# Kernel tuning notes

Hardware: AMD Instinct MI355X
Metric: run time of the kernel (lower is better)

The kernel has to match this reference:

```python
import jax, jax.numpy as jnp
import numpy as np

N_STEPS = 8


def _step(state, qop, dz_sub, W1, b1, W2, b2, W3, b3, W4, b4):
    # state [B,4], qop [B,1], dz_sub [B,1] -> residual-updated state [B,4]
    inp = jnp.concatenate([state, qop, dz_sub], axis=-1)  # [B,6]
    h = jax.nn.silu(inp @ W1 + b1)
    h = jax.nn.silu(h @ W2 + b2)
    h = jax.nn.silu(h @ W3 + b3)
    return state + (h @ W4 + b4)


def setup_inputs() -> dict:
    key = jax.random.key(0)
    ks = jax.random.split(key, 8)
    B = 262144
    H = 256
    # scale weights like xavier-ish init so activations stay sane
    def w(k, shape):
        fan_in = shape[0]
        return jax.random.normal(k, shape, dtype=jnp.float32) * (1.0 / np.sqrt(fan_in))
    state_dz = jax.random.normal(ks[0], (B, 6), dtype=jnp.float32)
    z_frac = jax.random.uniform(ks[1], (B,), dtype=jnp.float32)
    return {
        "state_dz": state_dz,
        "z_frac": z_frac,
        "W1": w(ks[2], (6, H)), "b1": jnp.zeros((H,), jnp.float32),
        "W2": w(ks[3], (H, H)), "b2": jnp.zeros((H,), jnp.float32),
        "W3": w(ks[4], (H, H)), "b3": jnp.zeros((H,), jnp.float32),
        "W4": w(ks[5], (H, 4)) * 0.1, "b4": jnp.zeros((4,), jnp.float32),
    }


def reference(state_dz, z_frac, W1, b1, W2, b2, W3, b3, W4, b4):
    # Faithful translation of CompositionalPINN.forward with z_frac of shape [B].
    # Torch uses max_steps = n_full.max().item() (host sync); running all N_STEPS
    # with the per-sample mask (n_full > step) yields identical math, since the
    # mask is 0 for step >= n_full.
    state = state_dz[:, :4]
    qop = state_dz[:, 4:5]
    dz_total = state_dz[:, 5:6]
    dz_sub = dz_total / N_STEPS

    continuous_steps = z_frac * N_STEPS            # [B]
    n_full = jnp.floor(continuous_steps)           # [B], kept float (compared vs step)
    frac_partial = continuous_steps - n_full       # [B]

    for step in range(N_STEPS):
        mask = (n_full > step).astype(state.dtype)[:, None]  # [B,1]
        new_state = _step(state, qop, dz_sub, W1, b1, W2, b2, W3, b3, W4, b4)
        state = mask * new_state + (1.0 - mask) * state

    dz_partial = frac_partial[:, None] * dz_sub
    has_partial = (frac_partial > 1e-6).astype(state.dtype)[:, None]
    partial_state = _step(state, qop, dz_partial, W1, b1, W2, b2, W3, b3, W4, b4)
    state = has_partial * partial_state + (1.0 - has_partial) * state
    return state
```

## Files before the change

kernel.cpp:

```cpp
#include <hip/hip_runtime.h>

typedef unsigned short u16;
typedef unsigned int u32;
typedef __attribute__((ext_vector_type(8))) short v8s;
typedef __attribute__((ext_vector_type(4))) float f32x4;

#define RPB 64
#define THREADS 256
#define NSB 512
#define W1F 0
#define W2F 8192
#define W3F 73728
#define W4F 139264
#define TOTW 143360
#define BH_OFF 286720
#define PERM_OFF 305152

#define MFMA(w, b, c) __builtin_amdgcn_mfma_f32_16x16x32_bf16((w), (b), (c), 0, 0, 0)

typedef __attribute__((address_space(1))) const unsigned int gu32;
typedef __attribute__((address_space(3))) unsigned int su32;
__device__ __forceinline__ void gld16(const u16* g, u16* l) {
  __builtin_amdgcn_global_load_lds((gu32*)g, (su32*)l, 16, 0, 0);
}

__device__ __forceinline__ u32 pk2(float a, float b) {
  u32 r;
  asm("v_cvt_pk_bf16_f32 %0, %1, %2" : "=v"(r) : "v"(a), "v"(b));
  return r;
}
__device__ __forceinline__ float bfu(u32 w, int hi) {
  return __uint_as_float(hi ? (w & 0xffff0000u) : (w << 16));
}
__device__ __forceinline__ f32x4 silu4(f32x4 v) {
  f32x4 r;
#pragma unroll
  for (int i = 0; i < 4; ++i) r[i] = v[i] * __builtin_amdgcn_rcpf(1.0f + __expf(-v[i]));
  return r;
}

__global__ void prep_weights(const float* __restrict__ W1, const float* __restrict__ W2,
                             const float* __restrict__ W3, const float* __restrict__ W4,
                             u16* __restrict__ Wf) {
  int e = blockIdx.x * 256 + threadIdx.x;
  if (e >= TOTW) return;
  float val = 0.0f;
  if (e < W2F) {
    int mt = e >> 9, idx = e & 511, l = idx >> 3, j = idx & 7;
    int q = l >> 4, m = l & 15;
    int f = 16 * (j >> 2) + 4 * q + (j & 3);
    int col = mt * 16 + m;
    val = (f < 6) ? W1[f * 256 + col] : ((f < 12) ? W1[(f - 6) * 256 + col] : 0.0f);
  } else if (e < W3F) {
    int e2 = e - W2F, blk = e2 >> 9, idx = e2 & 511, l = idx >> 3, j = idx & 7;
    int ks = blk >> 4, mt = blk & 15, q = l >> 4, m = l & 15;
    int f = 32 * ks + 16 * (j >> 2) + 4 * q + (j & 3);
    val = W2[f * 256 + mt * 16 + m];
  } else if (e < W4F) {
    int e2 = e - W3F, blk = e2 >> 9, idx = e2 & 511, l = idx >> 3, j = idx & 7;
    int ks = blk >> 4, mt = blk & 15, q = l >> 4, m = l & 15;
    int f = 32 * ks + 16 * (j >> 2) + 4 * q + (j & 3);
    val = W3[f * 256 + mt * 16 + m];
  } else {
    int e2 = e - W4F, ks = e2 >> 9, idx = e2 & 511, l = idx >> 3, j = idx & 7;
    int q = l >> 4, m = l & 15;
    int f = 32 * ks + 16 * (j >> 2) + 4 * q + (j & 3);
    val = (m < 4) ? W4[f * 4 + m] : 0.0f;
  }
  Wf[e] = (u16)pk2(val, val);
}

__global__ void hist_blocks(const float* __restrict__ zf, int* __restrict__ bh, int B) {
  __shared__ int h[9];
  int t = threadIdx.x;
  if (t < 9) h[t] = 0;
  __syncthreads();
  int r = blockIdx.x * 512 + t;
  if (r < B) {
    int nf = min(max((int)floorf(zf[r] * 8.0f), 0), 8);
    atomicAdd(&h[nf], 1);
  }
  __syncthreads();
  if (t < 9) bh[blockIdx.x * 9 + t] = h[t];
}

__global__ void scan_offsets(int* __restrict__ bh) {
  __shared__ int S[NSB * 9];
  __shared__ int tot[9], ebase[9];
  int t = threadIdx.x;
  for (int i = t; i < NSB * 9; i += 512) S[i] = bh[i];
  __syncthreads();
  if (t < 9) {
    int s = 0;
    for (int b = 0; b < NSB; ++b) s += S[b * 9 + t];
    tot[t] = s;
  }
  __syncthreads();
  if (t == 0) {
    int s = 0;
    for (int i = 0; i < 9; ++i) { ebase[i] = s; s += tot[i]; }
  }
  __syncthreads();
  if (t < 9) {
    int off = ebase[t];
    for (int b = 0; b < NSB; ++b) { int c = S[b * 9 + t]; S[b * 9 + t] = off; off += c; }
  }
  __syncthreads();
  for (int i = t; i < NSB * 9; i += 512) bh[i] = S[i];
}

__global__ void scatter_sorted(const float* __restrict__ zf, const int* __restrict__ bh,
                               int* __restrict__ perm, int B) {
  __shared__ int off[9];
  int t = threadIdx.x;
  if (t < 9) off[t] = bh[blockIdx.x * 9 + t];
  __syncthreads();
  int r = blockIdx.x * 512 + t;
  if (r < B) {
    int nf = min(max((int)floorf(zf[r] * 8.0f), 0), 8);
    int pos = atomicAdd(&off[nf], 1);
    perm[pos] = r;
  }
}

__global__ __attribute__((amdgpu_flat_work_group_size(256, 256)))
__attribute__((amdgpu_waves_per_eu(2, 2))) void pinn_main(
    const float* __restrict__ sdz, const float* __restrict__ zf,
    const u16* __restrict__ Wf, const int* __restrict__ perm,
    const float* __restrict__ b1, const float* __restrict__ b2,
    const float* __restrict__ b3, const float* __restrict__ b4,
    float* __restrict__ out) {
  __shared__ __align__(16) u16 ringS[4][4096];
  __shared__ __align__(16) u16 W1s[8192];
  __shared__ __align__(16) u16 W4s[4096];
  __shared__ __align__(16) float biasS[784];
  __shared__ __align__(16) float stS[RPB * 4];
  __shared__ float qopS[RPB], dzS[RPB], fracS[RPB];
  __shared__ int nfS[RPB], rowG[RPB];

  const int t = threadIdx.x;
  const int lane = t & 63;
  const int q = lane >> 4;
  const int n = lane & 15;
  const int wv = t >> 6;
  const int rb = wv * 16;

  if (t < RPB) {
    int rg = perm[blockIdx.x * RPB + t];
    rowG[t] = rg;
    const float* p = sdz + (size_t)rg * 6;
    stS[t * 4 + 0] = p[0]; stS[t * 4 + 1] = p[1];
    stS[t * 4 + 2] = p[2]; stS[t * 4 + 3] = p[3];
    qopS[t] = p[4];
    dzS[t] = p[5] * 0.125f;
    float cs = zf[rg] * 8.0f;
    float nfl = floorf(cs);
    nfS[t] = (int)nfl;
    fracS[t] = cs - nfl;
  }
  biasS[t] = b1[t]; biasS[256 + t] = b2[t]; biasS[512 + t] = b3[t];
  if (t < 16) biasS[768 + t] = (t < 4) ? b4[t] : 0.0f;
#pragma unroll
  for (int c = 0; c < 4; ++c)
    gld16(Wf + W1F + (c * 4 + wv) * 512 + lane * 8, &W1s[(c * 4 + wv) * 512]);
#pragma unroll
  for (int c = 0; c < 2; ++c)
    gld16(Wf + W4F + (c * 4 + wv) * 512 + lane * 8, &W4s[(c * 4 + wv) * 512]);
  __syncthreads();
  const int maxnf = nfS[RPB - 1];

  f32x4 acc[16];
  v8s bact[8];

#define ISSUE_HALF(AP)                                                        \
  do {                                                                        \
    int p_ = (AP) & 31;                                                       \
    int off_ = ((p_ >> 4) ? W3F : W2F) + ((p_ >> 1) & 7) * 8192 + (p_ & 1) * 4096; \
    u16* dst_ = &ringS[(AP) & 3][0];                                          \
    gld16(Wf + off_ + (2 * wv) * 512 + lane * 8, dst_ + (2 * wv) * 512);      \
    gld16(Wf + off_ + (2 * wv + 1) * 512 + lane * 8, dst_ + (2 * wv + 1) * 512); \
  } while (0)

  int ap = 0;
  ISSUE_HALF(ap);
  ISSUE_HALF(ap + 1);

#define PACK_BACT()                                              \
  do {                                                           \
    _Pragma("unroll") for (int ks = 0; ks < 8; ++ks) {           \
      f32x4 a0 = silu4(acc[2 * ks]);                             \
      f32x4 a1 = silu4(acc[2 * ks + 1]);                         \
      union { int4 i; v8s s; } u_;                               \
      u_.i.x = (int)pk2(a0[0], a0[1]);                           \
      u_.i.y = (int)pk2(a0[2], a0[3]);                           \
      u_.i.z = (int)pk2(a1[0], a1[1]);                           \
      u_.i.w = (int)pk2(a1[2], a1[3]);                           \
      bact[ks] = u_.s;                                           \
    }                                                            \
  } while (0)

  for (int ev = 0; ev <= maxnf; ++ev) {
    const bool partial = (ev == maxnf);

    v8s b1f;
    {
      const int row = rb + n;
      const float4 st = *(const float4*)&stS[row * 4];
      const float qop = qopS[row];
      const float dzv = partial ? fracS[row] * dzS[row] : dzS[row];
      u32 h01 = pk2(st.x, st.y), h23 = pk2(st.z, st.w), hqd = pk2(qop, dzv);
      float l0 = st.x - bfu(h01, 0), l1 = st.y - bfu(h01, 1);
      float l2 = st.z - bfu(h23, 0), l3 = st.w - bfu(h23, 1);
      float lq = qop - bfu(hqd, 0), ld = dzv - bfu(hqd, 1);
      u32 w0 = 0, w1 = 0;
      if (q == 0) { w0 = h01; w1 = h23; }
      else if (q == 1) { w0 = hqd; w1 = pk2(l0, l1); }
      else if (q == 2) { w0 = pk2(l2, l3); w1 = pk2(lq, ld); }
      union { int4 i; v8s s; } u_;
      u_.i.x = (int)w0; u_.i.y = (int)w1; u_.i.z = 0; u_.i.w = 0;
      b1f = u_.s;
    }

#pragma unroll
    for (int mt = 0; mt < 16; ++mt) {
      const v8s w = *(const v8s*)&W1s[mt * 512 + lane * 8];
      const float4 bb = *(const float4*)&biasS[mt * 16 + q * 4];
      const f32x4 binit = {bb.x, bb.y, bb.z, bb.w};
      acc[mt] = MFMA(w, b1f, binit);
    }
    PACK_BACT();

#pragma unroll
    for (int layer = 0; layer < 2; ++layer) {
      const int Lb = (layer == 0) ? 256 : 512;
#pragma unroll
      for (int mt = 0; mt < 16; ++mt) {
        const float4 bb = *(const float4*)&biasS[Lb + mt * 16 + q * 4];
        const f32x4 binit = {bb.x, bb.y, bb.z, bb.w};
        acc[mt] = binit;
      }
#pragma unroll
      for (int ks = 0; ks < 8; ++ks) {
#pragma unroll
        for (int h = 0; h < 2; ++h) {
          ISSUE_HALF(ap + 2);
          asm volatile("s_waitcnt vmcnt(4)" ::: "memory");
          __builtin_amdgcn_sched_barrier(0);
          __builtin_amdgcn_s_barrier();
          __builtin_amdgcn_sched_barrier(0);
          asm volatile("" ::: "memory");
          const u16* buf = &ringS[ap & 3][0];
          __builtin_amdgcn_s_setprio(1);
#pragma unroll
          for (int i = 0; i < 8; ++i) {
            const v8s w = *(const v8s*)&buf[i * 512 + lane * 8];
            acc[h * 8 + i] = MFMA(w, bact[ks], acc[h * 8 + i]);
          }
          __builtin_amdgcn_s_setprio(0);
          ++ap;
        }
      }
      PACK_BACT();
    }

    {
      const float4 bb = *(const float4*)&biasS[768 + q * 4];
      f32x4 a4 = {bb.x, bb.y, bb.z, bb.w};
#pragma unroll
      for (int ks = 0; ks < 8; ++ks) {
        const v8s w = *(const v8s*)&W4s[ks * 512 + lane * 8];
        a4 = MFMA(w, bact[ks], a4);
      }
      if (q == 0) {
        const int row = rb + n;
        const bool act = partial ? (fracS[row] > 1e-6f) : (nfS[row] > ev);
        if (act) {
          float4 cur = *(float4*)&stS[row * 4];
          cur.x += a4[0]; cur.y += a4[1];
          cur.z += a4[2]; cur.w += a4[3];
          *(float4*)&stS[row * 4] = cur;
        }
      }
    }
  }
  __syncthreads();

  {
    const int i = t;
    out[(size_t)rowG[i >> 2] * 4 + (i & 3)] = stS[i];
  }
}

extern "C" void kernel_launch(void* const* d_in, const int* in_sizes, int n_in,
                              void* d_out, int out_size, void* d_ws, size_t ws_size,
                              hipStream_t stream) {
  const float* sdz = (const float*)d_in[0];
  const float* zfr = (const float*)d_in[1];
  const float* W1 = (const float*)d_in[2];
  const float* b1 = (const float*)d_in[3];
  const float* W2 = (const float*)d_in[4];
  const float* b2 = (const float*)d_in[5];
  const float* W3 = (const float*)d_in[6];
  const float* b3 = (const float*)d_in[7];
  const float* W4 = (const float*)d_in[8];
  const float* b4 = (const float*)d_in[9];

  char* ws = (char*)d_ws;
  u16* Wf = (u16*)ws;
  int* bh = (int*)(ws + BH_OFF);
  int* perm = (int*)(ws + PERM_OFF);

  const int B = in_sizes[1];

  prep_weights<<<(TOTW + 255) / 256, 256, 0, stream>>>(W1, W2, W3, W4, Wf);
  hist_blocks<<<NSB, 512, 0, stream>>>(zfr, bh, B);
  scan_offsets<<<1, 512, 0, stream>>>(bh);
  scatter_sorted<<<NSB, 512, 0, stream>>>(zfr, bh, perm, B);
  pinn_main<<<B / RPB, THREADS, 0, stream>>>(sdz, zfr, Wf, perm, b1, b2, b3, b4,
                                             (float*)d_out);
}
```

Measured before the change: 549.8 us.

## Switch to 32x32x16 bf16 MFMA with 128 rows per block

```diff
diff --git a/kernel.cpp b/kernel.cpp
--- a/kernel.cpp
+++ b/kernel.cpp
@@ -3,20 +3,20 @@
 typedef unsigned short u16;
 typedef unsigned int u32;
 typedef __attribute__((ext_vector_type(8))) short v8s;
-typedef __attribute__((ext_vector_type(4))) float f32x4;
-
-#define RPB 64
+typedef __attribute__((ext_vector_type(16))) float f32x16;
+
+#define RPB 128
 #define THREADS 256
 #define NSB 512
 #define W1F 0
-#define W2F 8192
-#define W3F 73728
-#define W4F 139264
+#define W2F 4096
+#define W3F 69632
+#define W4F 135168
 #define TOTW 143360
 #define BH_OFF 286720
 #define PERM_OFF 305152
 
-#define MFMA(w, b, c) __builtin_amdgcn_mfma_f32_16x16x32_bf16((w), (b), (c), 0, 0, 0)
+#define MFMA32(w, b, c) __builtin_amdgcn_mfma_f32_32x32x16_bf16((w), (b), (c), 0, 0, 0)
 
 typedef __attribute__((address_space(1))) const unsigned int gu32;
 typedef __attribute__((address_space(3))) unsigned int su32;
@@ -32,11 +32,8 @@
 __device__ __forceinline__ float bfu(u32 w, int hi) {
   return __uint_as_float(hi ? (w & 0xffff0000u) : (w << 16));
 }
-__device__ __forceinline__ f32x4 silu4(f32x4 v) {
-  f32x4 r;
-#pragma unroll
-  for (int i = 0; i < 4; ++i) r[i] = v[i] * __builtin_amdgcn_rcpf(1.0f + __expf(-v[i]));
-  return r;
+__device__ __forceinline__ float silu1(float x) {
+  return x * __builtin_amdgcn_rcpf(1.0f + __expf(-x));
 }
 
 __global__ void prep_weights(const float* __restrict__ W1, const float* __restrict__ W2,
@@ -47,24 +44,24 @@
   float val = 0.0f;
   if (e < W2F) {
     int mt = e >> 9, idx = e & 511, l = idx >> 3, j = idx & 7;
-    int q = l >> 4, m = l & 15;
-    int f = 16 * (j >> 2) + 4 * q + (j & 3);
-    int col = mt * 16 + m;
+    int g = l >> 5, m = l & 31;
+    int f = ((j >> 2) << 3) + (g << 2) + (j & 3);
+    int col = mt * 32 + m;
     val = (f < 6) ? W1[f * 256 + col] : ((f < 12) ? W1[(f - 6) * 256 + col] : 0.0f);
   } else if (e < W3F) {
     int e2 = e - W2F, blk = e2 >> 9, idx = e2 & 511, l = idx >> 3, j = idx & 7;
-    int ks = blk >> 4, mt = blk & 15, q = l >> 4, m = l & 15;
-    int f = 32 * ks + 16 * (j >> 2) + 4 * q + (j & 3);
-    val = W2[f * 256 + mt * 16 + m];
+    int s = blk >> 3, mt = blk & 7, g = l >> 5, m = l & 31;
+    int f = ((s >> 1) << 5) + ((s & 1) << 4) + ((j >> 2) << 3) + (g << 2) + (j & 3);
+    val = W2[f * 256 + mt * 32 + m];
   } else if (e < W4F) {
     int e2 = e - W3F, blk = e2 >> 9, idx = e2 & 511, l = idx >> 3, j = idx & 7;
-    int ks = blk >> 4, mt = blk & 15, q = l >> 4, m = l & 15;
-    int f = 32 * ks + 16 * (j >> 2) + 4 * q + (j & 3);
-    val = W3[f * 256 + mt * 16 + m];
+    int s = blk >> 3, mt = blk & 7, g = l >> 5, m = l & 31;
+    int f = ((s >> 1) << 5) + ((s & 1) << 4) + ((j >> 2) << 3) + (g << 2) + (j & 3);
+    val = W3[f * 256 + mt * 32 + m];
   } else {
-    int e2 = e - W4F, ks = e2 >> 9, idx = e2 & 511, l = idx >> 3, j = idx & 7;
-    int q = l >> 4, m = l & 15;
-    int f = 32 * ks + 16 * (j >> 2) + 4 * q + (j & 3);
+    int e2 = e - W4F, s = e2 >> 9, idx = e2 & 511, l = idx >> 3, j = idx & 7;
+    int g = l >> 5, m = l & 31;
+    int f = ((s >> 1) << 5) + ((s & 1) << 4) + ((j >> 2) << 3) + (g << 2) + (j & 3);
     val = (m < 4) ? W4[f * 4 + m] : 0.0f;
   }
   Wf[e] = (u16)pk2(val, val);
@@ -131,19 +128,20 @@
     const float* __restrict__ b3, const float* __restrict__ b4,
     float* __restrict__ out) {
   __shared__ __align__(16) u16 ringS[4][4096];
-  __shared__ __align__(16) u16 W1s[8192];
-  __shared__ __align__(16) u16 W4s[4096];
-  __shared__ __align__(16) float biasS[784];
+  __shared__ __align__(16) u16 W1s[4096];
+  __shared__ __align__(16) u16 W4s[8192];
+  __shared__ __align__(16) float biasS[800];
   __shared__ __align__(16) float stS[RPB * 4];
   __shared__ float qopS[RPB], dzS[RPB], fracS[RPB];
   __shared__ int nfS[RPB], rowG[RPB];
 
   const int t = threadIdx.x;
   const int lane = t & 63;
-  const int q = lane >> 4;
-  const int n = lane & 15;
+  const int g = lane >> 5;
+  const int g4 = g << 2;
+  const int n32 = lane & 31;
   const int wv = t >> 6;
-  const int rb = wv * 16;
+  const int rb = wv * 32;
 
   if (t < RPB) {
     int rg = perm[blockIdx.x * RPB + t];
@@ -159,44 +157,60 @@
     fracS[t] = cs - nfl;
   }
   biasS[t] = b1[t]; biasS[256 + t] = b2[t]; biasS[512 + t] = b3[t];
-  if (t < 16) biasS[768 + t] = (t < 4) ? b4[t] : 0.0f;
+  if (t < 32) biasS[768 + t] = (t < 4) ? b4[t] : 0.0f;
+#pragma unroll
+  for (int c = 0; c < 2; ++c)
+    gld16(Wf + W1F + (c * 4 + wv) * 512 + lane * 8, &W1s[(c * 4 + wv) * 512]);
 #pragma unroll
   for (int c = 0; c < 4; ++c)
-    gld16(Wf + W1F + (c * 4 + wv) * 512 + lane * 8, &W1s[(c * 4 + wv) * 512]);
-#pragma unroll
-  for (int c = 0; c < 2; ++c)
     gld16(Wf + W4F + (c * 4 + wv) * 512 + lane * 8, &W4s[(c * 4 + wv) * 512]);
   __syncthreads();
   const int maxnf = nfS[RPB - 1];
 
-  f32x4 acc[16];
-  v8s bact[8];
-
-#define ISSUE_HALF(AP)                                                        \
+  f32x16 acc[8];
+  v8s bact[16];
+
+#define ISSUE_SLICE(AP)                                                       \
   do {                                                                        \
     int p_ = (AP) & 31;                                                       \
-    int off_ = ((p_ >> 4) ? W3F : W2F) + ((p_ >> 1) & 7) * 8192 + (p_ & 1) * 4096; \
+    int off_ = ((p_ >> 4) ? W3F : W2F) + (p_ & 15) * 4096;                    \
     u16* dst_ = &ringS[(AP) & 3][0];                                          \
     gld16(Wf + off_ + (2 * wv) * 512 + lane * 8, dst_ + (2 * wv) * 512);      \
     gld16(Wf + off_ + (2 * wv + 1) * 512 + lane * 8, dst_ + (2 * wv + 1) * 512); \
   } while (0)
 
   int ap = 0;
-  ISSUE_HALF(ap);
-  ISSUE_HALF(ap + 1);
-
-#define PACK_BACT()                                              \
-  do {                                                           \
-    _Pragma("unroll") for (int ks = 0; ks < 8; ++ks) {           \
-      f32x4 a0 = silu4(acc[2 * ks]);                             \
-      f32x4 a1 = silu4(acc[2 * ks + 1]);                         \
-      union { int4 i; v8s s; } u_;                               \
-      u_.i.x = (int)pk2(a0[0], a0[1]);                           \
-      u_.i.y = (int)pk2(a0[2], a0[3]);                           \
-      u_.i.z = (int)pk2(a1[0], a1[1]);                           \
-      u_.i.w = (int)pk2(a1[2], a1[3]);                           \
-      bact[ks] = u_.s;                                           \
-    }                                                            \
+  ISSUE_SLICE(ap);
+  ISSUE_SLICE(ap + 1);
+
+#define PACK_BACT()                                                 \
+  do {                                                              \
+    _Pragma("unroll") for (int mt = 0; mt < 8; ++mt) {              \
+      float s_[16];                                                 \
+      _Pragma("unroll") for (int i = 0; i < 16; ++i)                \
+          s_[i] = silu1(acc[mt][i]);                                \
+      union { int4 i4; v8s v; } lo_, hi_;                           \
+      lo_.i4.x = (int)pk2(s_[0], s_[1]);                            \
+      lo_.i4.y = (int)pk2(s_[2], s_[3]);                            \
+      lo_.i4.z = (int)pk2(s_[4], s_[5]);                            \
+      lo_.i4.w = (int)pk2(s_[6], s_[7]);                            \
+      hi_.i4.x = (int)pk2(s_[8], s_[9]);                            \
+      hi_.i4.y = (int)pk2(s_[10], s_[11]);                          \
+      hi_.i4.z = (int)pk2(s_[12], s_[13]);                          \
+      hi_.i4.w = (int)pk2(s_[14], s_[15]);                          \
+      bact[2 * mt] = lo_.v;                                         \
+      bact[2 * mt + 1] = hi_.v;                                     \
+    }                                                               \
+  } while (0)
+
+#define BINIT(BI, LB, MT)                                           \
+  do {                                                              \
+    _Pragma("unroll") for (int rq = 0; rq < 4; ++rq) {              \
+      const float4 bb =                                             \
+          *(const float4*)&biasS[(LB) + (MT) * 32 + rq * 8 + g4];   \
+      (BI)[4 * rq + 0] = bb.x; (BI)[4 * rq + 1] = bb.y;             \
+      (BI)[4 * rq + 2] = bb.z; (BI)[4 * rq + 3] = bb.w;             \
+    }                                                               \
   } while (0)
 
   for (int ev = 0; ev <= maxnf; ++ev) {
@@ -204,7 +218,7 @@
 
     v8s b1f;
     {
-      const int row = rb + n;
+      const int row = rb + n32;
       const float4 st = *(const float4*)&stS[row * 4];
       const float qop = qopS[row];
       const float dzv = partial ? fracS[row] * dzS[row] : dzS[row];
@@ -212,21 +226,23 @@
       float l0 = st.x - bfu(h01, 0), l1 = st.y - bfu(h01, 1);
       float l2 = st.z - bfu(h23, 0), l3 = st.w - bfu(h23, 1);
       float lq = qop - bfu(hqd, 0), ld = dzv - bfu(hqd, 1);
-      u32 w0 = 0, w1 = 0;
-      if (q == 0) { w0 = h01; w1 = h23; }
-      else if (q == 1) { w0 = hqd; w1 = pk2(l0, l1); }
-      else if (q == 2) { w0 = pk2(l2, l3); w1 = pk2(lq, ld); }
-      union { int4 i; v8s s; } u_;
-      u_.i.x = (int)w0; u_.i.y = (int)w1; u_.i.z = 0; u_.i.w = 0;
-      b1f = u_.s;
+      union { int4 i4; v8s v; } u_;
+      if (g == 0) {
+        u_.i4.x = (int)h01; u_.i4.y = (int)h23;
+        u_.i4.z = (int)pk2(l2, l3); u_.i4.w = (int)pk2(lq, ld);
+      } else {
+        u_.i4.x = (int)hqd; u_.i4.y = (int)pk2(l0, l1);
+        u_.i4.z = 0; u_.i4.w = 0;
+      }
+      b1f = u_.v;
     }
 
 #pragma unroll
-    for (int mt = 0; mt < 16; ++mt) {
+    for (int mt = 0; mt < 8; ++mt) {
       const v8s w = *(const v8s*)&W1s[mt * 512 + lane * 8];
-      const float4 bb = *(const float4*)&biasS[mt * 16 + q * 4];
-      const f32x4 binit = {bb.x, bb.y, bb.z, bb.w};
-      acc[mt] = MFMA(w, b1f, binit);
+      f32x16 bi;
+      BINIT(bi, 0, mt);
+      acc[mt] = MFMA32(w, b1f, bi);
     }
     PACK_BACT();
 
@@ -234,45 +250,47 @@
     for (int layer = 0; layer < 2; ++layer) {
       const int Lb = (layer == 0) ? 256 : 512;
 #pragma unroll
-      for (int mt = 0; mt < 16; ++mt) {
-        const float4 bb = *(const float4*)&biasS[Lb + mt * 16 + q * 4];
-        const f32x4 binit = {bb.x, bb.y, bb.z, bb.w};
-        acc[mt] = binit;
-      }
-#pragma unroll
-      for (int ks = 0; ks < 8; ++ks) {
-#pragma unroll
-        for (int h = 0; h < 2; ++h) {
-          ISSUE_HALF(ap + 2);
-          asm volatile("s_waitcnt vmcnt(4)" ::: "memory");
-          __builtin_amdgcn_sched_barrier(0);
-          __builtin_amdgcn_s_barrier();
-          __builtin_amdgcn_sched_barrier(0);
-          asm volatile("" ::: "memory");
-          const u16* buf = &ringS[ap & 3][0];
-          __builtin_amdgcn_s_setprio(1);
-#pragma unroll
-          for (int i = 0; i < 8; ++i) {
-            const v8s w = *(const v8s*)&buf[i * 512 + lane * 8];
-            acc[h * 8 + i] = MFMA(w, bact[ks], acc[h * 8 + i]);
-          }
-          __builtin_amdgcn_s_setprio(0);
-          ++ap;
+      for (int mt = 0; mt < 8; ++mt) {
+        f32x16 bi;
+        BINIT(bi, Lb, mt);
+        acc[mt] = bi;
+      }
+#pragma unroll
+      for (int s = 0; s < 16; ++s) {
+        ISSUE_SLICE(ap + 2);
+        asm volatile("s_waitcnt vmcnt(4)" ::: "memory");
+        __builtin_amdgcn_sched_barrier(0);
+        __builtin_amdgcn_s_barrier();
+        __builtin_amdgcn_sched_barrier(0);
+        asm volatile("" ::: "memory");
+        const u16* buf = &ringS[ap & 3][0];
+        __builtin_amdgcn_s_setprio(1);
+#pragma unroll
+        for (int mt = 0; mt < 8; ++mt) {
+          const v8s w = *(const v8s*)&buf[mt * 512 + lane * 8];
+          acc[mt] = MFMA32(w, bact[s], acc[mt]);
         }
+        __builtin_amdgcn_s_setprio(0);
+        ++ap;
       }
       PACK_BACT();
     }
 
     {
-      const float4 bb = *(const float4*)&biasS[768 + q * 4];
-      f32x4 a4 = {bb.x, bb.y, bb.z, bb.w};
-#pragma unroll
-      for (int ks = 0; ks < 8; ++ks) {
-        const v8s w = *(const v8s*)&W4s[ks * 512 + lane * 8];
-        a4 = MFMA(w, bact[ks], a4);
-      }
-      if (q == 0) {
-        const int row = rb + n;
+      f32x16 a4;
+#pragma unroll
+      for (int rq = 0; rq < 4; ++rq) {
+        const float4 bb = *(const float4*)&biasS[768 + rq * 8 + g4];
+        a4[4 * rq + 0] = bb.x; a4[4 * rq + 1] = bb.y;
+        a4[4 * rq + 2] = bb.z; a4[4 * rq + 3] = bb.w;
+      }
+#pragma unroll
+      for (int s = 0; s < 16; ++s) {
+        const v8s w = *(const v8s*)&W4s[s * 512 + lane * 8];
+        a4 = MFMA32(w, bact[s], a4);
+      }
+      if (g == 0) {
+        const int row = rb + n32;
         const bool act = partial ? (fracS[row] > 1e-6f) : (nfS[row] > ev);
         if (act) {
           float4 cur = *(float4*)&stS[row * 4];
@@ -285,10 +303,9 @@
   }
   __syncthreads();
 
-  {
-    const int i = t;
+#pragma unroll
+  for (int i = t; i < RPB * 4; i += THREADS)
     out[(size_t)rowG[i >> 2] * 4 + (i & 3)] = stS[i];
-  }
 }
 
 extern "C" void kernel_launch(void* const* d_in, const int* in_sizes, int n_in,
```

Result: slower. 695.1 us (+26.4%).

## Fold layer-1 bias into MFMA and shrink LDS ring to raise occupancy

Applied to the files above, without the earlier changes.

```diff
diff --git a/kernel.cpp b/kernel.cpp
--- a/kernel.cpp
+++ b/kernel.cpp
@@ -39,9 +39,9 @@
   return r;
 }
 
-__global__ void prep_weights(const float* __restrict__ W1, const float* __restrict__ W2,
-                             const float* __restrict__ W3, const float* __restrict__ W4,
-                             u16* __restrict__ Wf) {
+__global__ void prep_weights(const float* __restrict__ W1, const float* __restrict__ b1,
+                             const float* __restrict__ W2, const float* __restrict__ W3,
+                             const float* __restrict__ W4, u16* __restrict__ Wf) {
   int e = blockIdx.x * 256 + threadIdx.x;
   if (e >= TOTW) return;
   float val = 0.0f;
@@ -50,7 +50,9 @@
     int q = l >> 4, m = l & 15;
     int f = 16 * (j >> 2) + 4 * q + (j & 3);
     int col = mt * 16 + m;
-    val = (f < 6) ? W1[f * 256 + col] : ((f < 12) ? W1[(f - 6) * 256 + col] : 0.0f);
+    val = (f < 6) ? W1[f * 256 + col]
+        : ((f < 12) ? W1[(f - 6) * 256 + col]
+        : ((f == 12) ? b1[col] : 0.0f));
   } else if (e < W3F) {
     int e2 = e - W2F, blk = e2 >> 9, idx = e2 & 511, l = idx >> 3, j = idx & 7;
     int ks = blk >> 4, mt = blk & 15, q = l >> 4, m = l & 15;
@@ -124,16 +126,15 @@
 }
 
 __global__ __attribute__((amdgpu_flat_work_group_size(256, 256)))
-__attribute__((amdgpu_waves_per_eu(2, 2))) void pinn_main(
+__attribute__((amdgpu_waves_per_eu(3, 3))) void pinn_main(
     const float* __restrict__ sdz, const float* __restrict__ zf,
     const u16* __restrict__ Wf, const int* __restrict__ perm,
-    const float* __restrict__ b1, const float* __restrict__ b2,
-    const float* __restrict__ b3, const float* __restrict__ b4,
-    float* __restrict__ out) {
-  __shared__ __align__(16) u16 ringS[4][4096];
+    const float* __restrict__ b2, const float* __restrict__ b3,
+    const float* __restrict__ b4, float* __restrict__ out) {
+  __shared__ __align__(16) u16 ringS[3][4096];
   __shared__ __align__(16) u16 W1s[8192];
   __shared__ __align__(16) u16 W4s[4096];
-  __shared__ __align__(16) float biasS[784];
+  __shared__ __align__(16) float biasS[528];
   __shared__ __align__(16) float stS[RPB * 4];
   __shared__ float qopS[RPB], dzS[RPB], fracS[RPB];
   __shared__ int nfS[RPB], rowG[RPB];
@@ -158,8 +159,8 @@
     nfS[t] = (int)nfl;
     fracS[t] = cs - nfl;
   }
-  biasS[t] = b1[t]; biasS[256 + t] = b2[t]; biasS[512 + t] = b3[t];
-  if (t < 16) biasS[768 + t] = (t < 4) ? b4[t] : 0.0f;
+  biasS[t] = b2[t]; biasS[256 + t] = b3[t];
+  if (t < 16) biasS[512 + t] = (t < 4) ? b4[t] : 0.0f;
 #pragma unroll
   for (int c = 0; c < 4; ++c)
     gld16(Wf + W1F + (c * 4 + wv) * 512 + lane * 8, &W1s[(c * 4 + wv) * 512]);
@@ -171,19 +172,20 @@
 
   f32x4 acc[16];
   v8s bact[8];
-
-#define ISSUE_HALF(AP)                                                        \
+  const f32x4 Z4 = {0.0f, 0.0f, 0.0f, 0.0f};
+
+#define ISSUE_HALF(AP, BUF)                                                   \
   do {                                                                        \
     int p_ = (AP) & 31;                                                       \
     int off_ = ((p_ >> 4) ? W3F : W2F) + ((p_ >> 1) & 7) * 8192 + (p_ & 1) * 4096; \
-    u16* dst_ = &ringS[(AP) & 3][0];                                          \
+    u16* dst_ = &ringS[(BUF)][0];                                             \
     gld16(Wf + off_ + (2 * wv) * 512 + lane * 8, dst_ + (2 * wv) * 512);      \
     gld16(Wf + off_ + (2 * wv + 1) * 512 + lane * 8, dst_ + (2 * wv + 1) * 512); \
   } while (0)
 
   int ap = 0;
-  ISSUE_HALF(ap);
-  ISSUE_HALF(ap + 1);
+  int bc = 0;
+  ISSUE_HALF(0, 0);
 
 #define PACK_BACT()                                              \
   do {                                                           \
@@ -216,6 +218,7 @@
       if (q == 0) { w0 = h01; w1 = h23; }
       else if (q == 1) { w0 = hqd; w1 = pk2(l0, l1); }
       else if (q == 2) { w0 = pk2(l2, l3); w1 = pk2(lq, ld); }
+      else { w0 = 0x00003F80u; }
       union { int4 i; v8s s; } u_;
       u_.i.x = (int)w0; u_.i.y = (int)w1; u_.i.z = 0; u_.i.w = 0;
       b1f = u_.s;
@@ -224,15 +227,13 @@
 #pragma unroll
     for (int mt = 0; mt < 16; ++mt) {
       const v8s w = *(const v8s*)&W1s[mt * 512 + lane * 8];
-      const float4 bb = *(const float4*)&biasS[mt * 16 + q * 4];
-      const f32x4 binit = {bb.x, bb.y, bb.z, bb.w};
-      acc[mt] = MFMA(w, b1f, binit);
+      acc[mt] = MFMA(w, b1f, Z4);
     }
     PACK_BACT();
 
 #pragma unroll
     for (int layer = 0; layer < 2; ++layer) {
-      const int Lb = (layer == 0) ? 256 : 512;
+      const int Lb = (layer == 0) ? 0 : 256;
 #pragma unroll
       for (int mt = 0; mt < 16; ++mt) {
         const float4 bb = *(const float4*)&biasS[Lb + mt * 16 + q * 4];
@@ -243,13 +244,14 @@
       for (int ks = 0; ks < 8; ++ks) {
 #pragma unroll
         for (int h = 0; h < 2; ++h) {
-          ISSUE_HALF(ap + 2);
-          asm volatile("s_waitcnt vmcnt(4)" ::: "memory");
+          int bn = bc + 1; if (bn == 3) bn = 0;
+          ISSUE_HALF(ap + 1, bn);
+          asm volatile("s_waitcnt vmcnt(2)" ::: "memory");
           __builtin_amdgcn_sched_barrier(0);
           __builtin_amdgcn_s_barrier();
           __builtin_amdgcn_sched_barrier(0);
           asm volatile("" ::: "memory");
-          const u16* buf = &ringS[ap & 3][0];
+          const u16* buf = &ringS[bc][0];
           __builtin_amdgcn_s_setprio(1);
 #pragma unroll
           for (int i = 0; i < 8; ++i) {
@@ -257,14 +259,14 @@
             acc[h * 8 + i] = MFMA(w, bact[ks], acc[h * 8 + i]);
           }
           __builtin_amdgcn_s_setprio(0);
-          ++ap;
+          bc = bn; ++ap;
         }
       }
       PACK_BACT();
     }
 
     {
-      const float4 bb = *(const float4*)&biasS[768 + q * 4];
+      const float4 bb = *(const float4*)&biasS[512 + q * 4];
       f32x4 a4 = {bb.x, bb.y, bb.z, bb.w};
 #pragma unroll
       for (int ks = 0; ks < 8; ++ks) {
@@ -312,10 +314,10 @@
 
   const int B = in_sizes[1];
 
-  prep_weights<<<(TOTW + 255) / 256, 256, 0, stream>>>(W1, W2, W3, W4, Wf);
+  prep_weights<<<(TOTW + 255) / 256, 256, 0, stream>>>(W1, b1, W2, W3, W4, Wf);
   hist_blocks<<<NSB, 512, 0, stream>>>(zfr, bh, B);
   scan_offsets<<<1, 512, 0, stream>>>(bh);
   scatter_sorted<<<NSB, 512, 0, stream>>>(zfr, bh, perm, B);
-  pinn_main<<<B / RPB, THREADS, 0, stream>>>(sdz, zfr, Wf, perm, b1, b2, b3, b4,
+  pinn_main<<<B / RPB, THREADS, 0, stream>>>(sdz, zfr, Wf, perm, b2, b3, b4,
                                              (float*)d_out);
 }
```

New measurement: 843.0 us. 53.3% more time.
